# Optimization experiments

Measured on AMD Instinct MI355X. Metric: run time of the kernel, lower is better.

The kernel has to match this reference:

```python
import jax, jax.numpy as jnp
import numpy as np
from jax import lax

H = 512
W = 512
KS = 9  # dilation and Gaussian kernel size
# OpenCV: sigma=0 -> sigma = 0.3*((ksize-1)*0.5 - 1) + 0.8 = 1.7 for ksize=9
_SIGMA = 0.3 * ((KS - 1) * 0.5 - 1.0) + 0.8
_g = np.exp(-0.5 * ((np.arange(KS) - (KS - 1) / 2.0) / _SIGMA) ** 2)
_g = (_g / _g.sum()).astype(np.float32)
GAUSS = jnp.asarray(_g)


def setup_inputs() -> dict:
    key = jax.random.key(0)
    k1, k2, k3 = jax.random.split(key, 3)
    B, N = 64, 13860
    eye = jnp.eye(4, dtype=jnp.float32)
    # near-identity camera matrices so points project on-screen
    V = eye + 0.02 * jax.random.normal(k1, (B, 4, 4), jnp.float32)
    P = eye + 0.02 * jax.random.normal(k2, (B, 4, 4), jnp.float32)
    xyz = jax.random.uniform(k3, (N, 3), jnp.float32, -0.9, 0.9)
    pts = jnp.concatenate([xyz, jnp.ones((N, 1), jnp.float32)], axis=1)
    return {"V_matrix": V, "P_matrix": P, "raw_base_points": pts}


def reference(V_matrix, P_matrix, raw_base_points):
    B = V_matrix.shape[0]
    VP = jnp.einsum('bij,bjk->bik', P_matrix, V_matrix)          # [B,4,4]
    tp = jnp.einsum('ni,bji->bnj', raw_base_points, VP)          # points @ VP^T -> [B,N,4]
    w = tp[..., 3:4]
    xyz = jnp.where(w != 0, tp[..., :3] / w, tp[..., :3])       # perspective divide
    sx = jnp.round((xyz[..., 0] + 1.0) * 0.5 * W).astype(jnp.int32)
    sy = jnp.round((1.0 - (xyz[..., 1] + 1.0) * 0.5) * H).astype(jnp.int32)
    valid = (sx >= 0) & (sx < W) & (sy >= 0) & (sy < H)
    flat = jnp.where(valid, sy * W + sx, -1)                     # -1 -> dropped by scatter

    def splat(f):  # point splat: 255 at hit pixels (this is the inverted image)
        return jnp.zeros(H * W, jnp.float32).at[f].set(255.0, mode='drop').reshape(H, W)

    img = jax.vmap(splat)(flat)                                  # [B,H,W] in {0,255}
    dil = lax.reduce_window(img, -jnp.inf, lax.max, (1, KS, KS), (1, 1, 1), 'SAME')
    # 9x9 Gaussian blur, separable, BORDER_REFLECT_101 (OpenCV default)
    pad = jnp.pad(dil, ((0, 0), (KS // 2, KS // 2), (KS // 2, KS // 2)), mode='reflect')
    x = pad[:, None]                                             # [B,1,H+8,W+8]
    sm = lax.conv_general_dilated(x, GAUSS.reshape(1, 1, KS, 1), (1, 1), 'VALID')
    sm = lax.conv_general_dilated(sm, GAUSS.reshape(1, 1, 1, KS), (1, 1), 'VALID')[:, 0]
    # threshold(smoothed > 100) -> 255, then /255 -> {0,1}
    mask = (jnp.round(sm) > 100.0).astype(jnp.float32)           # [B,H,W]
    return jnp.broadcast_to(mask[:, None], (B, 3, H, W))
```

## Files before the change

kernel.cpp:

```cpp
#include <hip/hip_runtime.h>
#include <math.h>
#include <stdint.h>

#define HH 512
#define WW 512
#define BB 64
#define NP 13860
#define WPR 16
#define IMG_WORDS (BB * HH * WPR)

struct GaussW { float g[9]; };

__device__ __forceinline__ int reflect_idx(int i) {
    if (i < 0) i = -i;
    if (i > 511) i = 1022 - i;
    return i;
}

__global__ __launch_bounds__(256)
void zero_kernel(uint4* __restrict__ p) {
    p[blockIdx.x * 256 + threadIdx.x] = make_uint4(0u, 0u, 0u, 0u);
}

__global__ __launch_bounds__(256)
void splat_kernel(const float* __restrict__ V,
                  const float* __restrict__ P,
                  const float* __restrict__ pts,
                  unsigned int* __restrict__ gbm) {
    __shared__ float VP[4][4];
    const int b = blockIdx.y;
    const int t = threadIdx.x;
    if (t < 16) {
        const int i = t >> 2, k = t & 3;
        const float* Pb = P + b * 16;
        const float* Vb = V + b * 16;
        float a = __fmul_rn(Pb[i*4+0], Vb[0*4+k]);
        a = __fmaf_rn(Pb[i*4+1], Vb[1*4+k], a);
        a = __fmaf_rn(Pb[i*4+2], Vb[2*4+k], a);
        a = __fmaf_rn(Pb[i*4+3], Vb[3*4+k], a);
        VP[i][k] = a;
    }
    __syncthreads();
    const int n = blockIdx.x * 256 + t;
    if (n >= NP) return;
    const float4 p = ((const float4*)pts)[n];
    float tp0, tp1, tp3;
    {
        float a = __fmul_rn(p.x, VP[0][0]);
        a = __fmaf_rn(p.y, VP[0][1], a);
        a = __fmaf_rn(p.z, VP[0][2], a);
        a = __fmaf_rn(p.w, VP[0][3], a);
        tp0 = a;
    }
    {
        float a = __fmul_rn(p.x, VP[1][0]);
        a = __fmaf_rn(p.y, VP[1][1], a);
        a = __fmaf_rn(p.z, VP[1][2], a);
        a = __fmaf_rn(p.w, VP[1][3], a);
        tp1 = a;
    }
    {
        float a = __fmul_rn(p.x, VP[3][0]);
        a = __fmaf_rn(p.y, VP[3][1], a);
        a = __fmaf_rn(p.z, VP[3][2], a);
        a = __fmaf_rn(p.w, VP[3][3], a);
        tp3 = a;
    }
    const float w = tp3;
    const float x = (w != 0.f) ? (tp0 / w) : tp0;
    const float y = (w != 0.f) ? (tp1 / w) : tp1;
    const float sxf = rintf(__fmul_rn(__fmul_rn(__fadd_rn(x, 1.f), 0.5f), 512.f));
    const float tmp = __fmul_rn(__fadd_rn(y, 1.f), 0.5f);
    const float syf = rintf(__fmul_rn(__fsub_rn(1.f, tmp), 512.f));
    int sx, sy;
    if (sxf >= 0.f && sxf < 512.f && syf >= 0.f && syf < 512.f) {
        sx = (int)sxf; sy = (int)syf;
    } else {
        sx = 511; sy = 511;
    }
    atomicOr(&gbm[(b * HH + sy) * WPR + (sx >> 5)], 1u << (sx & 31));
}

__global__ __launch_bounds__(256)
void tile_kernel(const unsigned int* __restrict__ gbm,
                 float* __restrict__ out, GaussW gw) {
    __shared__ unsigned int hd[80][4];
    __shared__ unsigned int dl[72][4];
    __shared__ float lut[512];

    const int b  = blockIdx.z;
    const int x0 = blockIdx.x * 64;
    const int y0 = blockIdx.y * 64;
    const int tx = threadIdx.x;
    const int ty = threadIdx.y;
    const int tid = ty * 16 + tx;

    const int R0  = (y0 - 8 > 0) ? y0 - 8 : 0;
    const int R1  = (y0 + 71 < 511) ? y0 + 71 : 511;
    const int W0  = (x0 == 0) ? 0 : (x0 / 32 - 1);
    const int RD0 = (y0 - 4 > 0) ? y0 - 4 : 0;
    const int RD1 = (y0 + 67 < 511) ? y0 + 67 : 511;
    const int NR  = R1 - R0 + 1;

    for (int e = tid; e < 512; e += 256) {
        float acc = 0.f;
#pragma unroll
        for (int dy = 0; dy < 9; ++dy) {
            const float val = ((e >> dy) & 1) ? 255.f : 0.f;
            acc = __fmaf_rn(gw.g[dy], val, acc);
        }
        lut[e] = acc;
    }

    const unsigned int* gb = gbm + b * HH * WPR;
    for (int e = tid; e < NR * 4; e += 256) {
        const int r = e >> 2, j = e & 3;
        const int gr = R0 + r, gj = W0 + j;
        const unsigned int w  = (gj < WPR)              ? gb[gr * WPR + gj]     : 0u;
        const unsigned int wl = (gj > 0 && gj - 1 < WPR) ? gb[gr * WPR + gj - 1] : 0u;
        const unsigned int wr = (gj + 1 < WPR)           ? gb[gr * WPR + gj + 1] : 0u;
        unsigned int h = w;
#pragma unroll
        for (int k = 1; k <= 4; ++k) {
            h |= (w << k) | (wl >> (32 - k));
            h |= (w >> k) | (wr << (32 - k));
        }
        hd[r][j] = h;
    }
    __syncthreads();

    const int ND = RD1 - RD0 + 1;
    for (int e = tid; e < ND * 4; e += 256) {
        const int r = RD0 + (e >> 2), j = e & 3;
        const int lo = (r - 4 > 0) ? r - 4 : 0;
        const int hi = (r + 4 < 511) ? r + 4 : 511;
        unsigned int acc = 0u;
        for (int rr = lo; rr <= hi; ++rr) acc |= hd[rr - R0][j];
        dl[r - RD0][j] = acc;
    }
    __syncthreads();

    const int c0 = 4 * tx;
    int rrk[12];
    const int rbase = y0 + 4 * ty - 4;
#pragma unroll
    for (int k = 0; k < 12; ++k)
        rrk[k] = reflect_idx(rbase + k) - RD0;

    const int colA = reflect_idx(x0 + c0 - 4);
    const int colB = reflect_idx(x0 + c0 + 7);
    const int wA = (colA >> 5) - W0;
    const int wB = (colB >> 5) - W0;
    const bool colRef = (x0 == 0 && tx == 0) || (x0 == 448 && tx == 15);

    unsigned int v12[12];
    if (!colRef) {
        const int sh = colA & 31;
        unsigned int e12[12];
#pragma unroll
        for (int k = 0; k < 12; ++k) {
            const unsigned long long cat =
                (((unsigned long long)dl[rrk[k]][wB]) << 32) |
                (unsigned long long)dl[rrk[k]][wA];
            e12[k] = (unsigned int)(cat >> sh) & 0xFFFu;
        }
#pragma unroll
        for (int j = 0; j < 12; ++j) {
            unsigned int v = 0u;
#pragma unroll
            for (int k = 0; k < 12; ++k)
                v |= ((e12[k] >> j) & 1u) << k;
            v12[j] = v;
        }
    } else {
#pragma unroll
        for (int j = 0; j < 12; ++j) {
            const int col = reflect_idx(x0 + c0 - 4 + j);
            const int sel = (col >> 5) - W0;
            const int shc = col & 31;
            unsigned int v = 0u;
#pragma unroll
            for (int k = 0; k < 12; ++k)
                v |= ((dl[rrk[k]][sel] >> shc) & 1u) << k;
            v12[j] = v;
        }
    }

#pragma unroll
    for (int r = 0; r < 4; ++r) {
        float f[12];
#pragma unroll
        for (int j = 0; j < 12; ++j)
            f[j] = lut[(v12[j] >> r) & 0x1FFu];
        float4 mq;
        float* mp = (float*)&mq;
#pragma unroll
        for (int q = 0; q < 4; ++q) {
            float acc = 0.f;
#pragma unroll
            for (int dx = 0; dx < 9; ++dx)
                acc = __fmaf_rn(gw.g[dx], f[q + dx], acc);
            mp[q] = (rintf(acc) > 100.f) ? 1.f : 0.f;
        }
        const int yq = y0 + 4 * ty + r, xq = x0 + c0;
        float* o = out + ((size_t)(b * 3) * HH + yq) * WW + xq;
        *(float4*)(o)                       = mq;
        *(float4*)(o + (size_t)HH * WW)     = mq;
        *(float4*)(o + (size_t)2 * HH * WW) = mq;
    }
}

extern "C" void kernel_launch(void* const* d_in, const int* in_sizes, int n_in,
                              void* d_out, int out_size, void* d_ws, size_t ws_size,
                              hipStream_t stream) {
    const float* V   = (const float*)d_in[0];
    const float* P   = (const float*)d_in[1];
    const float* pts = (const float*)d_in[2];
    float* out = (float*)d_out;
    unsigned int* gbm = (unsigned int*)d_ws;

    const double sigma = 0.3 * ((9 - 1) * 0.5 - 1.0) + 0.8;
    double gd[9];
    for (int i = 0; i < 9; ++i) {
        const double t = ((double)i - 4.0) / sigma;
        gd[i] = exp(-0.5 * (t * t));
    }
    double s = ((gd[0] + gd[1]) + (gd[2] + gd[3])) + ((gd[4] + gd[5]) + (gd[6] + gd[7]));
    s += gd[8];
    GaussW gw;
    for (int i = 0; i < 9; ++i) gw.g[i] = (float)(gd[i] / s);

    zero_kernel<<<IMG_WORDS / 4 / 256, 256, 0, stream>>>((uint4*)gbm);
    splat_kernel<<<dim3((NP + 255) / 256, BB), 256, 0, stream>>>(V, P, pts, gbm);
    tile_kernel<<<dim3(8, 8, BB), dim3(16, 16), 0, stream>>>(gbm, out, gw);
}
```

Before: 90.44 us.

## Split dilation into global passes and skip blur for uniform neighborhoods

```diff
diff --git a/kernel.cpp b/kernel.cpp
--- a/kernel.cpp
+++ b/kernel.cpp
@@ -82,10 +82,41 @@
 }
 
 __global__ __launch_bounds__(256)
-void tile_kernel(const unsigned int* __restrict__ gbm,
+void hdil_kernel(const unsigned int* __restrict__ in,
+                 unsigned int* __restrict__ out) {
+    const int idx = blockIdx.x * 256 + threadIdx.x;
+    const int wx = idx & (WPR - 1);
+    const unsigned int w  = in[idx];
+    const unsigned int wl = (wx > 0)       ? in[idx - 1] : 0u;
+    const unsigned int wr = (wx < WPR - 1) ? in[idx + 1] : 0u;
+    unsigned int hd = w;
+#pragma unroll
+    for (int k = 1; k <= 4; ++k) {
+        hd |= (w << k) | (wl >> (32 - k));
+        hd |= (w >> k) | (wr << (32 - k));
+    }
+    out[idx] = hd;
+}
+
+__global__ __launch_bounds__(256)
+void vdil_kernel(const unsigned int* __restrict__ in,
+                 unsigned int* __restrict__ out) {
+    const int idx = blockIdx.x * 256 + threadIdx.x;
+    const int b   = idx / (HH * WPR);
+    const int rem = idx - b * (HH * WPR);
+    const int r   = rem >> 4;
+    const int wx  = rem & (WPR - 1);
+    const int lo = (r - 4 > 0) ? r - 4 : 0;
+    const int hi = (r + 4 < HH - 1) ? r + 4 : HH - 1;
+    const unsigned int* base = in + b * HH * WPR + wx;
+    unsigned int acc = 0u;
+    for (int rr = lo; rr <= hi; ++rr) acc |= base[rr * WPR];
+    out[idx] = acc;
+}
+
+__global__ __launch_bounds__(256)
+void tile_kernel(const unsigned int* __restrict__ gdil,
                  float* __restrict__ out, GaussW gw) {
-    __shared__ unsigned int hd[80][4];
-    __shared__ unsigned int dl[72][4];
     __shared__ float lut[512];
 
     const int b  = blockIdx.z;
@@ -95,13 +126,6 @@
     const int ty = threadIdx.y;
     const int tid = ty * 16 + tx;
 
-    const int R0  = (y0 - 8 > 0) ? y0 - 8 : 0;
-    const int R1  = (y0 + 71 < 511) ? y0 + 71 : 511;
-    const int W0  = (x0 == 0) ? 0 : (x0 / 32 - 1);
-    const int RD0 = (y0 - 4 > 0) ? y0 - 4 : 0;
-    const int RD1 = (y0 + 67 < 511) ? y0 + 67 : 511;
-    const int NR  = R1 - R0 + 1;
-
     for (int e = tid; e < 512; e += 256) {
         float acc = 0.f;
 #pragma unroll
@@ -111,96 +135,86 @@
         }
         lut[e] = acc;
     }
-
-    const unsigned int* gb = gbm + b * HH * WPR;
-    for (int e = tid; e < NR * 4; e += 256) {
-        const int r = e >> 2, j = e & 3;
-        const int gr = R0 + r, gj = W0 + j;
-        const unsigned int w  = (gj < WPR)              ? gb[gr * WPR + gj]     : 0u;
-        const unsigned int wl = (gj > 0 && gj - 1 < WPR) ? gb[gr * WPR + gj - 1] : 0u;
-        const unsigned int wr = (gj + 1 < WPR)           ? gb[gr * WPR + gj + 1] : 0u;
-        unsigned int h = w;
-#pragma unroll
-        for (int k = 1; k <= 4; ++k) {
-            h |= (w << k) | (wl >> (32 - k));
-            h |= (w >> k) | (wr << (32 - k));
-        }
-        hd[r][j] = h;
-    }
     __syncthreads();
 
-    const int ND = RD1 - RD0 + 1;
-    for (int e = tid; e < ND * 4; e += 256) {
-        const int r = RD0 + (e >> 2), j = e & 3;
-        const int lo = (r - 4 > 0) ? r - 4 : 0;
-        const int hi = (r + 4 < 511) ? r + 4 : 511;
-        unsigned int acc = 0u;
-        for (int rr = lo; rr <= hi; ++rr) acc |= hd[rr - R0][j];
-        dl[r - RD0][j] = acc;
-    }
-    __syncthreads();
-
+    const unsigned int* gb = gdil + b * HH * WPR;
     const int c0 = 4 * tx;
-    int rrk[12];
+
+    int rk[12];
     const int rbase = y0 + 4 * ty - 4;
 #pragma unroll
     for (int k = 0; k < 12; ++k)
-        rrk[k] = reflect_idx(rbase + k) - RD0;
-
-    const int colA = reflect_idx(x0 + c0 - 4);
-    const int colB = reflect_idx(x0 + c0 + 7);
-    const int wA = (colA >> 5) - W0;
-    const int wB = (colB >> 5) - W0;
+        rk[k] = reflect_idx(rbase + k) * WPR;
+
     const bool colRef = (x0 == 0 && tx == 0) || (x0 == 448 && tx == 15);
 
+    int mode = 2;
     unsigned int v12[12];
+
     if (!colRef) {
+        const int colA = x0 + c0 - 4;
+        const int wA = colA >> 5;
+        const int w2 = (wA + 1 < WPR) ? wA + 1 : WPR - 1;
         const int sh = colA & 31;
-        unsigned int e12[12];
+        unsigned int e12[12], fOr = 0u, fAnd = 0xFFFu;
 #pragma unroll
         for (int k = 0; k < 12; ++k) {
             const unsigned long long cat =
-                (((unsigned long long)dl[rrk[k]][wB]) << 32) |
-                (unsigned long long)dl[rrk[k]][wA];
+                (((unsigned long long)gb[rk[k] + w2]) << 32) |
+                (unsigned long long)gb[rk[k] + wA];
             e12[k] = (unsigned int)(cat >> sh) & 0xFFFu;
-        }
-#pragma unroll
-        for (int j = 0; j < 12; ++j) {
-            unsigned int v = 0u;
-#pragma unroll
-            for (int k = 0; k < 12; ++k)
-                v |= ((e12[k] >> j) & 1u) << k;
-            v12[j] = v;
+            fOr |= e12[k]; fAnd &= e12[k];
+        }
+        if (fOr == 0u)           mode = 0;
+        else if (fAnd == 0xFFFu) mode = 1;
+        else {
+#pragma unroll
+            for (int j = 0; j < 12; ++j) {
+                unsigned int v = 0u;
+#pragma unroll
+                for (int k = 0; k < 12; ++k)
+                    v |= ((e12[k] >> j) & 1u) << k;
+                v12[j] = v;
+            }
         }
     } else {
+        const int wsel = (x0 == 0) ? 0 : WPR - 1;
+        unsigned int d[12];
+#pragma unroll
+        for (int k = 0; k < 12; ++k) d[k] = gb[rk[k] + wsel];
 #pragma unroll
         for (int j = 0; j < 12; ++j) {
             const int col = reflect_idx(x0 + c0 - 4 + j);
-            const int sel = (col >> 5) - W0;
             const int shc = col & 31;
             unsigned int v = 0u;
 #pragma unroll
             for (int k = 0; k < 12; ++k)
-                v |= ((dl[rrk[k]][sel] >> shc) & 1u) << k;
+                v |= ((d[k] >> shc) & 1u) << k;
             v12[j] = v;
         }
     }
 
 #pragma unroll
     for (int r = 0; r < 4; ++r) {
-        float f[12];
-#pragma unroll
-        for (int j = 0; j < 12; ++j)
-            f[j] = lut[(v12[j] >> r) & 0x1FFu];
         float4 mq;
         float* mp = (float*)&mq;
-#pragma unroll
-        for (int q = 0; q < 4; ++q) {
-            float acc = 0.f;
-#pragma unroll
-            for (int dx = 0; dx < 9; ++dx)
-                acc = __fmaf_rn(gw.g[dx], f[q + dx], acc);
-            mp[q] = (rintf(acc) > 100.f) ? 1.f : 0.f;
+        if (mode == 0) {
+            mq = make_float4(0.f, 0.f, 0.f, 0.f);
+        } else if (mode == 1) {
+            mq = make_float4(1.f, 1.f, 1.f, 1.f);
+        } else {
+            float f[12];
+#pragma unroll
+            for (int j = 0; j < 12; ++j)
+                f[j] = lut[(v12[j] >> r) & 0x1FFu];
+#pragma unroll
+            for (int q = 0; q < 4; ++q) {
+                float acc = 0.f;
+#pragma unroll
+                for (int dx = 0; dx < 9; ++dx)
+                    acc = __fmaf_rn(gw.g[dx], f[q + dx], acc);
+                mp[q] = (rintf(acc) > 100.f) ? 1.f : 0.f;
+            }
         }
         const int yq = y0 + 4 * ty + r, xq = x0 + c0;
         float* o = out + ((size_t)(b * 3) * HH + yq) * WW + xq;
@@ -217,7 +231,8 @@
     const float* P   = (const float*)d_in[1];
     const float* pts = (const float*)d_in[2];
     float* out = (float*)d_out;
-    unsigned int* gbm = (unsigned int*)d_ws;
+    unsigned int* buf0 = (unsigned int*)d_ws;
+    unsigned int* buf1 = buf0 + IMG_WORDS;
 
     const double sigma = 0.3 * ((9 - 1) * 0.5 - 1.0) + 0.8;
     double gd[9];
@@ -230,7 +245,9 @@
     GaussW gw;
     for (int i = 0; i < 9; ++i) gw.g[i] = (float)(gd[i] / s);
 
-    zero_kernel<<<IMG_WORDS / 4 / 256, 256, 0, stream>>>((uint4*)gbm);
-    splat_kernel<<<dim3((NP + 255) / 256, BB), 256, 0, stream>>>(V, P, pts, gbm);
-    tile_kernel<<<dim3(8, 8, BB), dim3(16, 16), 0, stream>>>(gbm, out, gw);
-}
+    zero_kernel<<<IMG_WORDS / 4 / 256, 256, 0, stream>>>((uint4*)buf0);
+    splat_kernel<<<dim3((NP + 255) / 256, BB), 256, 0, stream>>>(V, P, pts, buf0);
+    hdil_kernel<<<IMG_WORDS / 256, 256, 0, stream>>>(buf0, buf1);
+    vdil_kernel<<<IMG_WORDS / 256, 256, 0, stream>>>(buf1, buf0);
+    tile_kernel<<<dim3(8, 8, BB), dim3(16, 16), 0, stream>>>(buf0, out, gw);
+}
```

After: 91.41 us. No clear change (+1.1%).

## Retile blur to wide row strips, skip uniform tiles, use nontemporal stores

Applied to the files above, without the earlier changes.

```diff
diff --git a/kernel.cpp b/kernel.cpp
--- a/kernel.cpp
+++ b/kernel.cpp
@@ -8,6 +8,10 @@
 #define NP 13860
 #define WPR 16
 #define IMG_WORDS (BB * HH * WPR)
+#define TW 256
+#define TH 16
+
+typedef float vfloat4 __attribute__((ext_vector_type(4)));
 
 struct GaussW { float g[9]; };
 
@@ -84,24 +88,32 @@
 __global__ __launch_bounds__(256)
 void tile_kernel(const unsigned int* __restrict__ gbm,
                  float* __restrict__ out, GaussW gw) {
-    __shared__ unsigned int hd[80][4];
-    __shared__ unsigned int dl[72][4];
+    __shared__ unsigned int bm[32][10];
+    __shared__ unsigned int hd[32][10];
+    __shared__ unsigned int dl[24][10];
     __shared__ float lut[512];
 
-    const int b  = blockIdx.z;
-    const int x0 = blockIdx.x * 64;
-    const int y0 = blockIdx.y * 64;
-    const int tx = threadIdx.x;
-    const int ty = threadIdx.y;
-    const int tid = ty * 16 + tx;
+    const int b   = blockIdx.z;
+    const int x0  = blockIdx.x * TW;
+    const int y0  = blockIdx.y * TH;
+    const int lx  = threadIdx.x;
+    const int tyq = threadIdx.y;
+    const int tid = tyq * 64 + lx;
 
     const int R0  = (y0 - 8 > 0) ? y0 - 8 : 0;
-    const int R1  = (y0 + 71 < 511) ? y0 + 71 : 511;
+    const int R1  = (y0 + TH + 7 < 511) ? y0 + TH + 7 : 511;
     const int W0  = (x0 == 0) ? 0 : (x0 / 32 - 1);
     const int RD0 = (y0 - 4 > 0) ? y0 - 4 : 0;
-    const int RD1 = (y0 + 67 < 511) ? y0 + 67 : 511;
+    const int RD1 = (y0 + TH + 3 < 511) ? y0 + TH + 3 : 511;
     const int NR  = R1 - R0 + 1;
 
+    const unsigned int* gb = gbm + b * HH * WPR;
+    for (int e = tid; e < 32 * 10; e += 256) {
+        const int r = e / 10, j = e - r * 10;
+        unsigned int v = 0u;
+        if (r < NR && W0 + j < WPR) v = gb[(R0 + r) * WPR + (W0 + j)];
+        bm[r][j] = v;
+    }
     for (int e = tid; e < 512; e += 256) {
         float acc = 0.f;
 #pragma unroll
@@ -111,14 +123,13 @@
         }
         lut[e] = acc;
     }
-
-    const unsigned int* gb = gbm + b * HH * WPR;
-    for (int e = tid; e < NR * 4; e += 256) {
-        const int r = e >> 2, j = e & 3;
-        const int gr = R0 + r, gj = W0 + j;
-        const unsigned int w  = (gj < WPR)              ? gb[gr * WPR + gj]     : 0u;
-        const unsigned int wl = (gj > 0 && gj - 1 < WPR) ? gb[gr * WPR + gj - 1] : 0u;
-        const unsigned int wr = (gj + 1 < WPR)           ? gb[gr * WPR + gj + 1] : 0u;
+    __syncthreads();
+
+    for (int e = tid; e < 32 * 10; e += 256) {
+        const int r = e / 10, j = e - r * 10;
+        const unsigned int w  = bm[r][j];
+        const unsigned int wl = (j > 0) ? bm[r][j-1] : 0u;
+        const unsigned int wr = (j < 9) ? bm[r][j+1] : 0u;
         unsigned int h = w;
 #pragma unroll
         for (int k = 1; k <= 4; ++k) {
@@ -129,84 +140,100 @@
     }
     __syncthreads();
 
-    const int ND = RD1 - RD0 + 1;
-    for (int e = tid; e < ND * 4; e += 256) {
-        const int r = RD0 + (e >> 2), j = e & 3;
-        const int lo = (r - 4 > 0) ? r - 4 : 0;
-        const int hi = (r + 4 < 511) ? r + 4 : 511;
+    for (int e = tid; e < 24 * 10; e += 256) {
+        const int r0 = e / 10, j = e - r0 * 10;
+        const int r = RD0 + r0;
         unsigned int acc = 0u;
-        for (int rr = lo; rr <= hi; ++rr) acc |= hd[rr - R0][j];
-        dl[r - RD0][j] = acc;
-    }
-    __syncthreads();
-
-    const int c0 = 4 * tx;
+        if (r <= RD1) {
+            const int lo = (r - 4 > 0) ? r - 4 : 0;
+            const int hi = (r + 4 < 511) ? r + 4 : 511;
+            for (int rr = lo; rr <= hi; ++rr) acc |= hd[rr - R0][j];
+        }
+        dl[r0][j] = acc;
+    }
+    __syncthreads();
+
+    const int c0 = 4 * lx;
     int rrk[12];
-    const int rbase = y0 + 4 * ty - 4;
+    const int rbase = y0 + 4 * tyq - 4;
 #pragma unroll
     for (int k = 0; k < 12; ++k)
         rrk[k] = reflect_idx(rbase + k) - RD0;
 
-    const int colA = reflect_idx(x0 + c0 - 4);
-    const int colB = reflect_idx(x0 + c0 + 7);
-    const int wA = (colA >> 5) - W0;
-    const int wB = (colB >> 5) - W0;
-    const bool colRef = (x0 == 0 && tx == 0) || (x0 == 448 && tx == 15);
-
+    const bool colRef = (x0 == 0 && lx == 0) || (x0 + TW == WW && lx == 63);
+    int mode = 2;
     unsigned int v12[12];
+
     if (!colRef) {
+        const int colA = x0 + c0 - 4;
+        const int wA = colA >> 5;
+        const int jA = wA - W0;
+        const int j2 = ((wA + 1 < WPR) ? wA + 1 : WPR - 1) - W0;
         const int sh = colA & 31;
-        unsigned int e12[12];
+        unsigned int e12[12], fOr = 0u, fAnd = 0xFFFu;
 #pragma unroll
         for (int k = 0; k < 12; ++k) {
             const unsigned long long cat =
-                (((unsigned long long)dl[rrk[k]][wB]) << 32) |
-                (unsigned long long)dl[rrk[k]][wA];
+                (((unsigned long long)dl[rrk[k]][j2]) << 32) |
+                (unsigned long long)dl[rrk[k]][jA];
             e12[k] = (unsigned int)(cat >> sh) & 0xFFFu;
-        }
-#pragma unroll
-        for (int j = 0; j < 12; ++j) {
-            unsigned int v = 0u;
-#pragma unroll
-            for (int k = 0; k < 12; ++k)
-                v |= ((e12[k] >> j) & 1u) << k;
-            v12[j] = v;
+            fOr |= e12[k]; fAnd &= e12[k];
+        }
+        if (fOr == 0u)           mode = 0;
+        else if (fAnd == 0xFFFu) mode = 1;
+        else {
+#pragma unroll
+            for (int j = 0; j < 12; ++j) {
+                unsigned int v = 0u;
+#pragma unroll
+                for (int k = 0; k < 12; ++k)
+                    v |= ((e12[k] >> j) & 1u) << k;
+                v12[j] = v;
+            }
         }
     } else {
+        const int jE = (x0 == 0) ? 0 : (WPR - 1 - W0);
+        unsigned int d[12];
+#pragma unroll
+        for (int k = 0; k < 12; ++k) d[k] = dl[rrk[k]][jE];
 #pragma unroll
         for (int j = 0; j < 12; ++j) {
             const int col = reflect_idx(x0 + c0 - 4 + j);
-            const int sel = (col >> 5) - W0;
             const int shc = col & 31;
             unsigned int v = 0u;
 #pragma unroll
             for (int k = 0; k < 12; ++k)
-                v |= ((dl[rrk[k]][sel] >> shc) & 1u) << k;
+                v |= ((d[k] >> shc) & 1u) << k;
             v12[j] = v;
         }
     }
 
 #pragma unroll
     for (int r = 0; r < 4; ++r) {
-        float f[12];
-#pragma unroll
-        for (int j = 0; j < 12; ++j)
-            f[j] = lut[(v12[j] >> r) & 0x1FFu];
-        float4 mq;
-        float* mp = (float*)&mq;
-#pragma unroll
-        for (int q = 0; q < 4; ++q) {
-            float acc = 0.f;
-#pragma unroll
-            for (int dx = 0; dx < 9; ++dx)
-                acc = __fmaf_rn(gw.g[dx], f[q + dx], acc);
-            mp[q] = (rintf(acc) > 100.f) ? 1.f : 0.f;
-        }
-        const int yq = y0 + 4 * ty + r, xq = x0 + c0;
-        float* o = out + ((size_t)(b * 3) * HH + yq) * WW + xq;
-        *(float4*)(o)                       = mq;
-        *(float4*)(o + (size_t)HH * WW)     = mq;
-        *(float4*)(o + (size_t)2 * HH * WW) = mq;
+        vfloat4 mq;
+        if (mode == 0) {
+            mq = (vfloat4)(0.f);
+        } else if (mode == 1) {
+            mq = (vfloat4)(1.f);
+        } else {
+            float f[12];
+#pragma unroll
+            for (int j = 0; j < 12; ++j)
+                f[j] = lut[(v12[j] >> r) & 0x1FFu];
+#pragma unroll
+            for (int q = 0; q < 4; ++q) {
+                float acc = 0.f;
+#pragma unroll
+                for (int dx = 0; dx < 9; ++dx)
+                    acc = __fmaf_rn(gw.g[dx], f[q + dx], acc);
+                mq[q] = (rintf(acc) > 100.f) ? 1.f : 0.f;
+            }
+        }
+        const int yq = y0 + 4 * tyq + r;
+        float* o = out + ((size_t)(b * 3) * HH + yq) * WW + x0 + c0;
+        __builtin_nontemporal_store(mq, (vfloat4*)(o));
+        __builtin_nontemporal_store(mq, (vfloat4*)(o + (size_t)HH * WW));
+        __builtin_nontemporal_store(mq, (vfloat4*)(o + (size_t)2 * HH * WW));
     }
 }
 
@@ -232,5 +259,5 @@
 
     zero_kernel<<<IMG_WORDS / 4 / 256, 256, 0, stream>>>((uint4*)gbm);
     splat_kernel<<<dim3((NP + 255) / 256, BB), 256, 0, stream>>>(V, P, pts, gbm);
-    tile_kernel<<<dim3(8, 8, BB), dim3(16, 16), 0, stream>>>(gbm, out, gw);
-}
+    tile_kernel<<<dim3(WW / TW, HH / TH, BB), dim3(64, 4), 0, stream>>>(gbm, out, gw);
+}
```

Measured after the change: 85.73 us. -5.2%, faster.
